# Kernel optimization log

Measured on AMD Instinct MI355X. Metric: run time of the kernel, lower is better.

The kernel has to match this reference:

```python
import jax, jax.numpy as jnp
import numpy as np


def exp_mix_frac(p1, p2, a1, b1, a2, b2):
    # stable merge of two (numerator, denominator) pairs carried in log-scale p
    p = jnp.maximum(p1, p2)
    e1 = jnp.exp(p1 - p)
    e2 = jnp.exp(p2 - p)
    return a1 * e1 + a2 * e2, b1 * e1 + b2 * e2, p


def assoc_reduce_step(left, right):
    akv_l, ak_l, w_l, p_l = left
    akv_r, ak_r, w_r, p_r = right
    a, b, p = exp_mix_frac(p_l + w_r, p_r, akv_l, ak_l, akv_r, ak_r)
    return a, b, w_l + w_r, p


def setup_inputs() -> dict:
    key = jax.random.key(0)
    ks = jax.random.split(key, 7)
    S, B, E = 2048, 8, 1024
    scale = 1.0 / np.sqrt(E)
    return {
        "x": jax.random.normal(ks[0], (S, B, E), jnp.float32),
        "tmrkv": jax.random.uniform(ks[1], (3 * E,), jnp.float32),
        "Wk": jax.random.normal(ks[2], (E, E), jnp.float32) * scale,
        "Wv": jax.random.normal(ks[3], (E, E), jnp.float32) * scale,
        "time_decay": jax.random.normal(ks[4], (E,), jnp.float32) - 1.0,
        "time_first": jax.random.normal(ks[5], (E,), jnp.float32),
        "Wout": jax.random.normal(ks[6], (E, E), jnp.float32) * scale,
    }


def reference(x, tmrkv, Wk, Wv, time_decay, time_first, Wout):
    # x: (S, B, E) time-major (batch_first=False path of the source module)
    S, B, E = x.shape
    x_prev = jnp.concatenate([jnp.zeros_like(x[:1]), x[:-1]], axis=0)
    # time_mix_rkv layout: [r | k | v]; r-branch is computed in the source but
    # never used in the associative-scan path, so it is omitted (same output).
    mk = tmrkv[E:2 * E]
    mv = tmrkv[2 * E:]
    k = (mk * x + (1.0 - mk) * x_prev) @ Wk  # (S, B, E)
    v = (mv * x + (1.0 - mv) * x_prev) @ Wv  # (S, B, E)

    k_ = k.reshape(S, B * E)
    v_ = v.reshape(S, B * E)
    W_ = jnp.broadcast_to(jnp.tile(time_decay, B)[None, :], (S, B * E))
    ones = jnp.ones_like(v_)
    # log-depth parallel scan over time with numerically-stable exp merge
    a_, b_, _, p_ = jax.lax.associative_scan(
        assoc_reduce_step, (v_, ones, W_, k_), axis=0)

    a_state = a_.reshape(S, B, E)
    b_state = b_.reshape(S, B, E)
    p_state = p_.reshape(S, B, E)
    c, d, _ = exp_mix_frac(p_state, k + time_first + time_decay,
                           a_state, b_state, v, jnp.ones_like(v))
    rwkv = c / d  # (S, B, E)
    return rwkv @ Wout
```

## Files before the change

### kernel.cpp

```cpp
#include <hip/hip_runtime.h>
#include <stdint.h>

#define S_LEN  2048
#define B_DIM  8
#define E_DIM  1024
#define BE     (B_DIM * E_DIM)
#define M_ROWS (S_LEN * B_DIM)
#define NCHUNK 64
#define CLEN   (S_LEN / NCHUNK)

typedef __attribute__((ext_vector_type(8))) short bf16x8;
typedef __attribute__((ext_vector_type(4))) float f32x4;

__device__ __forceinline__ unsigned short f2bf(float f) {
    unsigned int u = __float_as_uint(f);
    u += 0x7FFFu + ((u >> 16) & 1u);
    return (unsigned short)(u >> 16);
}
__device__ __forceinline__ float bf_lo(unsigned int u) {
    return __uint_as_float(u << 16);
}
__device__ __forceinline__ float bf_hi(unsigned int u) {
    return __uint_as_float(u & 0xFFFF0000u);
}

__global__ __launch_bounds__(256) void mix_kernel(
    const float* __restrict__ x, const float* __restrict__ tmrkv,
    unsigned short* __restrict__ xk, unsigned short* __restrict__ xv)
{
    int i = blockIdx.x * 256 + threadIdx.x;
    const float4* x4 = (const float4*)x;
    float4 xc[2], xp[2];
    xc[0] = x4[2 * i];
    xc[1] = x4[2 * i + 1];
    if (i >= BE / 8) {
        xp[0] = x4[2 * i - BE / 4];
        xp[1] = x4[2 * i + 1 - BE / 4];
    } else {
        xp[0] = make_float4(0.f, 0.f, 0.f, 0.f);
        xp[1] = make_float4(0.f, 0.f, 0.f, 0.f);
    }
    int e4 = (2 * i) & (E_DIM / 4 - 1);
    ushort4 ok[2], ov[2];
    #pragma unroll
    for (int h = 0; h < 2; ++h) {
        float4 mk = ((const float4*)(tmrkv + E_DIM))[e4 + h];
        float4 mv = ((const float4*)(tmrkv + 2 * E_DIM))[e4 + h];
        ok[h].x = f2bf(mk.x * xc[h].x + (1.f - mk.x) * xp[h].x);
        ok[h].y = f2bf(mk.y * xc[h].y + (1.f - mk.y) * xp[h].y);
        ok[h].z = f2bf(mk.z * xc[h].z + (1.f - mk.z) * xp[h].z);
        ok[h].w = f2bf(mk.w * xc[h].w + (1.f - mk.w) * xp[h].w);
        ov[h].x = f2bf(mv.x * xc[h].x + (1.f - mv.x) * xp[h].x);
        ov[h].y = f2bf(mv.y * xc[h].y + (1.f - mv.y) * xp[h].y);
        ov[h].z = f2bf(mv.z * xc[h].z + (1.f - mv.z) * xp[h].z);
        ov[h].w = f2bf(mv.w * xc[h].w + (1.f - mv.w) * xp[h].w);
    }
    ((ushort4*)xk)[2 * i]     = ok[0];
    ((ushort4*)xk)[2 * i + 1] = ok[1];
    ((ushort4*)xv)[2 * i]     = ov[0];
    ((ushort4*)xv)[2 * i + 1] = ov[1];
}

__global__ __launch_bounds__(256) void cast_transpose_k(
    const float* __restrict__ w0, const float* __restrict__ w1,
    const float* __restrict__ w2,
    unsigned short* __restrict__ o0, unsigned short* __restrict__ o1,
    unsigned short* __restrict__ o2)
{
    const float* in = blockIdx.z == 0 ? w0 : (blockIdx.z == 1 ? w1 : w2);
    unsigned short* out = blockIdx.z == 0 ? o0 : (blockIdx.z == 1 ? o1 : o2);
    __shared__ float tile[32][33];
    int bx = blockIdx.x * 32, by = blockIdx.y * 32;
    int tx = threadIdx.x, ty = threadIdx.y;
    #pragma unroll
    for (int i = 0; i < 32; i += 8)
        tile[ty + i][tx] = in[(size_t)(by + ty + i) * E_DIM + bx + tx];
    __syncthreads();
    #pragma unroll
    for (int i = 0; i < 32; i += 8)
        out[(size_t)(bx + ty + i) * E_DIM + by + tx] = f2bf(tile[tx][ty + i]);
}

#define BM 256
#define BN 256
#define BK 64

__device__ __forceinline__ void stage_plane(unsigned short* lds_base, int buf_plane,
                                            const unsigned short* gsrc, int K, int wave)
{
    #pragma unroll
    for (int s = 0; s < 2; ++s) {
        const unsigned short* g = gsrc + (size_t)s * 128 * K;
        unsigned short* l = lds_base + buf_plane * 8192 + s * 4096 + wave * 512;
        __builtin_amdgcn_global_load_lds(
            (const __attribute__((address_space(1))) unsigned int*)g,
            (__attribute__((address_space(3))) unsigned int*)l, 16, 0, 0);
    }
}

template <typename OutT>
__device__ __forceinline__ void gemm_body(
    const unsigned short* __restrict__ A,
    const unsigned short* __restrict__ BT,
    OutT* __restrict__ C, int M, int N, int K)
{
    __shared__ __align__(16) unsigned short smem[2][4][8192];
    const int tid  = threadIdx.x;
    const int wave = tid >> 6, lane = tid & 63;
    const int lrow = lane & 15, lq = lane >> 4;
    const int wm = wave >> 2, wn = wave & 3;
    const int bm = blockIdx.x * BM, bn = blockIdx.y * BN;

    const int srow = tid >> 2;
    const int sg   = (tid & 3) ^ ((srow >> 1) & 3);
    const unsigned short* sAp = A  + (size_t)(bm + srow) * K + sg * 8;
    const unsigned short* sBp = BT + (size_t)(bn + srow) * K + sg * 8;
    unsigned short* lb = &smem[0][0][0];

    f32x4 acc[8][4];
    #pragma unroll
    for (int i = 0; i < 8; ++i)
        #pragma unroll
        for (int j = 0; j < 4; ++j)
            acc[i][j] = (f32x4){0.f, 0.f, 0.f, 0.f};

    bf16x8 af[4], bfr[4];

#define LDA_(h, ib)                                                           \
    _Pragma("unroll")                                                         \
    for (int i = 0; i < 4; ++i) {                                             \
        int R = wm * 128 + ((ib) + i) * 16 + lrow;                            \
        af[i] = *(const bf16x8*)&smem[cur][(h) * 2]                           \
            [R * 32 + ((lq ^ ((R >> 1) & 3)) << 3)];                          \
    }
#define LDB_(h)                                                               \
    _Pragma("unroll")                                                         \
    for (int j = 0; j < 4; ++j) {                                             \
        int R = wn * 64 + j * 16 + lrow;                                      \
        bfr[j] = *(const bf16x8*)&smem[cur][(h) * 2 + 1]                      \
            [R * 32 + ((lq ^ ((R >> 1) & 3)) << 3)];                          \
    }
#define MMA_(ib)                                                              \
    __builtin_amdgcn_s_setprio(1);                                            \
    _Pragma("unroll")                                                         \
    for (int i = 0; i < 4; ++i)                                               \
        _Pragma("unroll")                                                     \
        for (int j = 0; j < 4; ++j)                                           \
            acc[(ib) + i][j] = __builtin_amdgcn_mfma_f32_16x16x32_bf16(       \
                af[i], bfr[j], acc[(ib) + i][j], 0, 0, 0);                    \
    __builtin_amdgcn_s_setprio(0);

    const int nk = K / BK;
    stage_plane(lb, 0, sAp,      K, wave);
    stage_plane(lb, 1, sBp,      K, wave);
    stage_plane(lb, 2, sAp + 32, K, wave);
    stage_plane(lb, 3, sBp + 32, K, wave);

    int cur = 0;
    for (int t = 0; t < nk - 1; ++t) {
        const int nxt = cur ^ 1;
        const unsigned short* nA = sAp + (size_t)(t + 1) * BK;
        const unsigned short* nB = sBp + (size_t)(t + 1) * BK;
        stage_plane(lb, nxt * 4 + 0, nA, K, wave);
        asm volatile("s_waitcnt vmcnt(6)" ::: "memory");
        __builtin_amdgcn_s_barrier();
        asm volatile("" ::: "memory");
        LDA_(0, 0); LDB_(0);
        MMA_(0);
        stage_plane(lb, nxt * 4 + 1, nB, K, wave);
        LDA_(0, 4);
        MMA_(4);
        stage_plane(lb, nxt * 4 + 2, nA + 32, K, wave);
        asm volatile("s_waitcnt vmcnt(6)" ::: "memory");
        __builtin_amdgcn_s_barrier();
        asm volatile("" ::: "memory");
        LDA_(1, 0); LDB_(1);
        MMA_(0);
        stage_plane(lb, nxt * 4 + 3, nB + 32, K, wave);
        LDA_(1, 4);
        asm volatile("s_waitcnt lgkmcnt(0)" ::: "memory");
        __builtin_amdgcn_s_barrier();
        asm volatile("" ::: "memory");
        MMA_(4);
        cur = nxt;
    }
    asm volatile("s_waitcnt vmcnt(4)" ::: "memory");
    __builtin_amdgcn_s_barrier();
    asm volatile("" ::: "memory");
    LDA_(0, 0); LDB_(0);
    MMA_(0);
    LDA_(0, 4);
    MMA_(4);
    asm volatile("s_waitcnt vmcnt(0)" ::: "memory");
    __builtin_amdgcn_s_barrier();
    asm volatile("" ::: "memory");
    LDA_(1, 0); LDB_(1);
    MMA_(0);
    LDA_(1, 4);
    MMA_(4);

    #pragma unroll
    for (int i = 0; i < 8; ++i)
        #pragma unroll
        for (int j = 0; j < 4; ++j)
            #pragma unroll
            for (int r = 0; r < 4; ++r) {
                int row = bm + wm * 128 + i * 16 + lq * 4 + r;
                int col = bn + wn * 64 + j * 16 + lrow;
                if constexpr (sizeof(OutT) == 2)
                    C[(size_t)row * N + col] = f2bf(acc[i][j][r]);
                else
                    C[(size_t)row * N + col] = acc[i][j][r];
            }
#undef LDA_
#undef LDB_
#undef MMA_
}

__global__ __launch_bounds__(512, 2) void gemm_kv(
    const unsigned short* __restrict__ A0, const unsigned short* __restrict__ B0,
    unsigned short* __restrict__ C0,
    const unsigned short* __restrict__ A1, const unsigned short* __restrict__ B1,
    unsigned short* __restrict__ C1, int M, int N, int K)
{
    if (blockIdx.z == 0) gemm_body<unsigned short>(A0, B0, C0, M, N, K);
    else                 gemm_body<unsigned short>(A1, B1, C1, M, N, K);
}

__global__ __launch_bounds__(512, 2) void gemm_out(
    const unsigned short* __restrict__ A, const unsigned short* __restrict__ BT,
    float* __restrict__ C, int M, int N, int K)
{
    gemm_body<float>(A, BT, C, M, N, K);
}

__device__ __forceinline__ void wkv_step(float& a, float& b, float& p,
                                         float kt, float vt, float w)
{
    float pw = p + w;
    float pn = fmaxf(pw, kt);
    float e1 = __expf(pw - pn), e2 = __expf(kt - pn);
    a = a * e1 + vt * e2;
    b = b * e1 + e2;
    p = pn;
}

#define Q_PER_T (BE / 4)

__global__ __launch_bounds__(256) void scan_pass1(
    const uint2* __restrict__ k4, const uint2* __restrict__ v4,
    const float* __restrict__ tdec,
    float4* __restrict__ sA, float4* __restrict__ sB, float4* __restrict__ sP)
{
    int g = blockIdx.x * 256 + threadIdx.x;
    int q = g & (Q_PER_T - 1);
    int c = g >> 11;
    float4 w4 = ((const float4*)tdec)[q & (E_DIM / 4 - 1)];
    size_t idx = (size_t)c * CLEN * Q_PER_T + q;
    uint2 ku = k4[idx], vu = v4[idx];
    float a0 = bf_lo(vu.x), b0 = 1.f, p0 = bf_lo(ku.x);
    float a1 = bf_hi(vu.x), b1 = 1.f, p1 = bf_hi(ku.x);
    float a2 = bf_lo(vu.y), b2 = 1.f, p2 = bf_lo(ku.y);
    float a3 = bf_hi(vu.y), b3 = 1.f, p3 = bf_hi(ku.y);
    for (int j = 1; j < CLEN; ++j) {
        idx += Q_PER_T;
        ku = k4[idx]; vu = v4[idx];
        wkv_step(a0, b0, p0, bf_lo(ku.x), bf_lo(vu.x), w4.x);
        wkv_step(a1, b1, p1, bf_hi(ku.x), bf_hi(vu.x), w4.y);
        wkv_step(a2, b2, p2, bf_lo(ku.y), bf_lo(vu.y), w4.z);
        wkv_step(a3, b3, p3, bf_hi(ku.y), bf_hi(vu.y), w4.w);
    }
    sA[g] = make_float4(a0, a1, a2, a3);
    sB[g] = make_float4(b0, b1, b2, b3);
    sP[g] = make_float4(p0, p1, p2, p3);
}

__global__ __launch_bounds__(256) void scan_pass2(
    const float* __restrict__ tdec,
    float* __restrict__ sA, float* __restrict__ sB, float* __restrict__ sP)
{
    __shared__ float tA[64 * 65], tB[64 * 65], tP[64 * 65];
    const int t   = threadIdx.x;
    const int ch0 = blockIdx.x * 64;
    const int chl = t & 63;
    const int cq  = t >> 6;
    #pragma unroll 4
    for (int cc = 0; cc < 16; ++cc) {
        int c = cq * 16 + cc;
        int idx = c * BE + ch0 + chl;
        tA[chl * 65 + c] = sA[idx];
        tB[chl * 65 + c] = sB[idx];
        tP[chl * 65 + c] = sP[idx];
    }
    __syncthreads();
    const int lane = t & 63, wave = t >> 6;
    for (int i = 0; i < 16; ++i) {
        int ch = wave * 16 + i;
        float w = tdec[(ch0 + ch) & (E_DIM - 1)];
        float a = tA[ch * 65 + lane];
        float b = tB[ch * 65 + lane];
        float p = tP[ch * 65 + lane];
        float W = (float)CLEN * w;
        #pragma unroll
        for (int d = 1; d < 64; d <<= 1) {
            float a_l = __shfl_up(a, d);
            float b_l = __shfl_up(b, d);
            float p_l = __shfl_up(p, d);
            float W_l = __shfl_up(W, d);
            if (lane >= d) {
                float pw = p_l + W;
                float pn = fmaxf(pw, p);
                float e1 = __expf(pw - pn), e2 = __expf(p - pn);
                a = a_l * e1 + a * e2;
                b = b_l * e1 + b * e2;
                p = pn;
                W = W_l + W;
            }
        }
        float ea = __shfl_up(a, 1);
        float eb = __shfl_up(b, 1);
        float ep = __shfl_up(p, 1);
        if (lane == 0) { ea = 0.f; eb = 0.f; ep = -__builtin_inff(); }
        tA[ch * 65 + lane] = ea;
        tB[ch * 65 + lane] = eb;
        tP[ch * 65 + lane] = ep;
    }
    __syncthreads();
    #pragma unroll 4
    for (int cc = 0; cc < 16; ++cc) {
        int c = cq * 16 + cc;
        int idx = c * BE + ch0 + chl;
        sA[idx] = tA[chl * 65 + c];
        sB[idx] = tB[chl * 65 + c];
        sP[idx] = tP[chl * 65 + c];
    }
}

__global__ __launch_bounds__(256) void scan_pass3(
    const uint2* __restrict__ k4, const uint2* __restrict__ v4,
    const float* __restrict__ tdec, const float* __restrict__ tfir,
    const float4* __restrict__ sA, const float4* __restrict__ sB,
    const float4* __restrict__ sP, uint2* __restrict__ rwkv4)
{
    int g = blockIdx.x * 256 + threadIdx.x;
    int q = g & (Q_PER_T - 1);
    int c = g >> 11;
    int e4 = q & (E_DIM / 4 - 1);
    float4 w4 = ((const float4*)tdec)[e4];
    float4 f4 = ((const float4*)tfir)[e4];
    float u0 = f4.x + w4.x, u1 = f4.y + w4.y;
    float u2 = f4.z + w4.z, u3 = f4.w + w4.w;
    float4 av = sA[g], bv = sB[g], pv = sP[g];
    float a0 = av.x, b0 = bv.x, p0 = pv.x;
    float a1 = av.y, b1 = bv.y, p1 = pv.y;
    float a2 = av.z, b2 = bv.z, p2 = pv.z;
    float a3 = av.w, b3 = bv.w, p3 = pv.w;
    size_t idx = (size_t)c * CLEN * Q_PER_T + q;
    for (int j = 0; j < CLEN; ++j) {
        uint2 ku = k4[idx], vu = v4[idx];
        float kt0 = bf_lo(ku.x), vt0 = bf_lo(vu.x);
        float kt1 = bf_hi(ku.x), vt1 = bf_hi(vu.x);
        float kt2 = bf_lo(ku.y), vt2 = bf_lo(vu.y);
        float kt3 = bf_hi(ku.y), vt3 = bf_hi(vu.y);
        wkv_step(a0, b0, p0, kt0, vt0, w4.x);
        wkv_step(a1, b1, p1, kt1, vt1, w4.y);
        wkv_step(a2, b2, p2, kt2, vt2, w4.z);
        wkv_step(a3, b3, p3, kt3, vt3, w4.w);
        float kb0 = kt0 + u0, kb1 = kt1 + u1, kb2 = kt2 + u2, kb3 = kt3 + u3;
        float q0 = fmaxf(p0, kb0), q1 = fmaxf(p1, kb1);
        float q2 = fmaxf(p2, kb2), q3 = fmaxf(p3, kb3);
        float g0 = __expf(p0 - q0), h0 = __expf(kb0 - q0);
        float g1 = __expf(p1 - q1), h1 = __expf(kb1 - q1);
        float g2 = __expf(p2 - q2), h2 = __expf(kb2 - q2);
        float g3 = __expf(p3 - q3), h3 = __expf(kb3 - q3);
        float r0 = (a0 * g0 + vt0 * h0) / (b0 * g0 + h0);
        float r1 = (a1 * g1 + vt1 * h1) / (b1 * g1 + h1);
        float r2 = (a2 * g2 + vt2 * h2) / (b2 * g2 + h2);
        float r3 = (a3 * g3 + vt3 * h3) / (b3 * g3 + h3);
        uint2 o;
        o.x = (unsigned int)f2bf(r0) | ((unsigned int)f2bf(r1) << 16);
        o.y = (unsigned int)f2bf(r2) | ((unsigned int)f2bf(r3) << 16);
        rwkv4[idx] = o;
        idx += Q_PER_T;
    }
}

extern "C" void kernel_launch(void* const* d_in, const int* in_sizes, int n_in,
                              void* d_out, int out_size, void* d_ws, size_t ws_size,
                              hipStream_t stream)
{
    const float* x     = (const float*)d_in[0];
    const float* tmrkv = (const float*)d_in[1];
    const float* Wk    = (const float*)d_in[2];
    const float* Wv    = (const float*)d_in[3];
    const float* tdec  = (const float*)d_in[4];
    const float* tfir  = (const float*)d_in[5];
    const float* Wout  = (const float*)d_in[6];
    float* out = (float*)d_out;

    char* ws = (char*)d_ws;
    const size_t SZ_BF = (size_t)M_ROWS * E_DIM * 2;
    unsigned short* xk   = (unsigned short*)(ws);
    unsigned short* xv   = (unsigned short*)(ws + SZ_BF);
    unsigned short* kbuf = (unsigned short*)(ws + 2 * SZ_BF);
    unsigned short* vbuf = (unsigned short*)(ws + 3 * SZ_BF);
    unsigned short* WkT  = (unsigned short*)(ws + 4 * SZ_BF);
    unsigned short* WvT  = WkT + (size_t)E_DIM * E_DIM;
    unsigned short* WoutT= WvT + (size_t)E_DIM * E_DIM;
    float* sA = (float*)xv;
    float* sB = sA + (size_t)NCHUNK * BE;
    float* sP = sB + (size_t)NCHUNK * BE;
    unsigned short* rwkv = xk;

    mix_kernel<<<(M_ROWS * E_DIM / 8) / 256, 256, 0, stream>>>(x, tmrkv, xk, xv);

    dim3 tb(32, 8), tg(E_DIM / 32, E_DIM / 32, 3);
    cast_transpose_k<<<tg, tb, 0, stream>>>(Wk, Wv, Wout, WkT, WvT, WoutT);

    dim3 gkv(M_ROWS / BM, E_DIM / BN, 2);
    gemm_kv<<<gkv, 512, 0, stream>>>(xk, WkT, kbuf, xv, WvT, vbuf,
                                     M_ROWS, E_DIM, E_DIM);

    scan_pass1<<<(NCHUNK * Q_PER_T) / 256, 256, 0, stream>>>(
        (const uint2*)kbuf, (const uint2*)vbuf, tdec,
        (float4*)sA, (float4*)sB, (float4*)sP);
    scan_pass2<<<BE / 64, 256, 0, stream>>>(tdec, sA, sB, sP);
    scan_pass3<<<(NCHUNK * Q_PER_T) / 256, 256, 0, stream>>>(
        (const uint2*)kbuf, (const uint2*)vbuf, tdec, tfir,
        (const float4*)sA, (const float4*)sB, (const float4*)sP,
        (uint2*)rwkv);

    dim3 gg(M_ROWS / BM, E_DIM / BN);
    gemm_out<<<gg, 512, 0, stream>>>(rwkv, WoutT, out, M_ROWS, E_DIM, E_DIM);
}
```

Baseline: 307.5 us.

## Switch GEMMs to 32x32x16 MFMA with XCD-aware block swizzle and reordered pipeline

The shared GEMM body now uses 32x32x16 bf16 MFMA instructions with 16-float accumulators instead of 16x16x32, which halves the number of LDS fragment loads per FLOP. The k-loop schedule is reordered so each gate (lgkm and vm wait plus barrier) comes before the LDS reads and the next-stage global loads are issued after them. Block indices are also remapped so that consecutive hardware block IDs on the same XCD cover neighbouring M tiles, which should improve L2 reuse. Together these aim to raise MFMA throughput and cache locality, at the cost of an extra full lgkmcnt wait per gate. The swizzle also hardcodes a grid of 64 M tiles per XCD group, which matches M=16384/256.

```diff
diff --git a/kernel.cpp b/kernel.cpp
--- a/kernel.cpp
+++ b/kernel.cpp
@@ -11,6 +11,7 @@
 
 typedef __attribute__((ext_vector_type(8))) short bf16x8;
 typedef __attribute__((ext_vector_type(4))) float f32x4;
+typedef __attribute__((ext_vector_type(16))) float f32x16;
 
 __device__ __forceinline__ unsigned short f2bf(float f) {
     unsigned int u = __float_as_uint(f);
@@ -98,18 +99,27 @@
     }
 }
 
+__device__ __forceinline__ void swz_xy(int& bx, int& by)
+{
+    int hw   = blockIdx.x + gridDim.x * blockIdx.y;
+    int xcd  = hw & 7;
+    int slot = hw >> 3;
+    bx = xcd * 8 + (slot & 7);
+    by = slot >> 3;
+}
+
 template <typename OutT>
 __device__ __forceinline__ void gemm_body(
     const unsigned short* __restrict__ A,
     const unsigned short* __restrict__ BT,
-    OutT* __restrict__ C, int M, int N, int K)
+    OutT* __restrict__ C, int M, int N, int K, int bxt, int byt)
 {
     __shared__ __align__(16) unsigned short smem[2][4][8192];
     const int tid  = threadIdx.x;
     const int wave = tid >> 6, lane = tid & 63;
-    const int lrow = lane & 15, lq = lane >> 4;
+    const int l31 = lane & 31, lh = lane >> 5;
     const int wm = wave >> 2, wn = wave & 3;
-    const int bm = blockIdx.x * BM, bn = blockIdx.y * BN;
+    const int bm = bxt * BM, bn = byt * BN;
 
     const int srow = tid >> 2;
     const int sg   = (tid & 3) ^ ((srow >> 1) & 3);
@@ -117,37 +127,55 @@
     const unsigned short* sBp = BT + (size_t)(bn + srow) * K + sg * 8;
     unsigned short* lb = &smem[0][0][0];
 
-    f32x4 acc[8][4];
-    #pragma unroll
-    for (int i = 0; i < 8; ++i)
+    f32x16 acc[4][2];
+    #pragma unroll
+    for (int i = 0; i < 4; ++i)
         #pragma unroll
-        for (int j = 0; j < 4; ++j)
-            acc[i][j] = (f32x4){0.f, 0.f, 0.f, 0.f};
-
-    bf16x8 af[4], bfr[4];
-
-#define LDA_(h, ib)                                                           \
+        for (int j = 0; j < 2; ++j)
+            #pragma unroll
+            for (int e = 0; e < 16; ++e)
+                acc[i][j][e] = 0.f;
+
+    bf16x8 af[2][2], bfr[2][2];
+
+#define GATE_(n)                                                              \
+    asm volatile("s_waitcnt lgkmcnt(0)" ::: "memory");                        \
+    asm volatile("s_waitcnt vmcnt(" #n ")" ::: "memory");                     \
+    __builtin_amdgcn_s_barrier();                                             \
+    asm volatile("" ::: "memory");
+
+#define LDA2_(h, mh)                                                          \
     _Pragma("unroll")                                                         \
-    for (int i = 0; i < 4; ++i) {                                             \
-        int R = wm * 128 + ((ib) + i) * 16 + lrow;                            \
-        af[i] = *(const bf16x8*)&smem[cur][(h) * 2]                           \
-            [R * 32 + ((lq ^ ((R >> 1) & 3)) << 3)];                          \
-    }
-#define LDB_(h)                                                               \
+    for (int ii = 0; ii < 2; ++ii)                                            \
+        _Pragma("unroll")                                                     \
+        for (int s = 0; s < 2; ++s) {                                         \
+            int R = wm * 128 + (2 * (mh) + ii) * 32 + l31;                    \
+            int g = s * 2 + lh;                                               \
+            af[ii][s] = *(const bf16x8*)&smem[cur][(h) * 2]                   \
+                [R * 32 + ((g ^ ((R >> 1) & 3)) << 3)];                       \
+        }
+#define LDB2_(h)                                                              \
     _Pragma("unroll")                                                         \
-    for (int j = 0; j < 4; ++j) {                                             \
-        int R = wn * 64 + j * 16 + lrow;                                      \
-        bfr[j] = *(const bf16x8*)&smem[cur][(h) * 2 + 1]                      \
-            [R * 32 + ((lq ^ ((R >> 1) & 3)) << 3)];                          \
-    }
-#define MMA_(ib)                                                              \
+    for (int jj = 0; jj < 2; ++jj)                                            \
+        _Pragma("unroll")                                                     \
+        for (int s = 0; s < 2; ++s) {                                         \
+            int R = wn * 64 + jj * 32 + l31;                                  \
+            int g = s * 2 + lh;                                               \
+            bfr[jj][s] = *(const bf16x8*)&smem[cur][(h) * 2 + 1]              \
+                [R * 32 + ((g ^ ((R >> 1) & 3)) << 3)];                       \
+        }
+#define MMA2_(mh)                                                             \
     __builtin_amdgcn_s_setprio(1);                                            \
     _Pragma("unroll")                                                         \
-    for (int i = 0; i < 4; ++i)                                               \
+    for (int ii = 0; ii < 2; ++ii)                                            \
         _Pragma("unroll")                                                     \
-        for (int j = 0; j < 4; ++j)                                           \
-            acc[(ib) + i][j] = __builtin_amdgcn_mfma_f32_16x16x32_bf16(       \
-                af[i], bfr[j], acc[(ib) + i][j], 0, 0, 0);                    \
+        for (int jj = 0; jj < 2; ++jj)                                        \
+            _Pragma("unroll")                                                 \
+            for (int s = 0; s < 2; ++s)                                       \
+                acc[2 * (mh) + ii][jj] =                                      \
+                    __builtin_amdgcn_mfma_f32_32x32x16_bf16(                  \
+                        af[ii][s], bfr[jj][s], acc[2 * (mh) + ii][jj],        \
+                        0, 0, 0);                                             \
     __builtin_amdgcn_s_setprio(0);
 
     const int nk = K / BK;
@@ -161,60 +189,50 @@
         const int nxt = cur ^ 1;
         const unsigned short* nA = sAp + (size_t)(t + 1) * BK;
         const unsigned short* nB = sBp + (size_t)(t + 1) * BK;
+        GATE_(4);
+        LDA2_(0, 0); LDB2_(0);
         stage_plane(lb, nxt * 4 + 0, nA, K, wave);
-        asm volatile("s_waitcnt vmcnt(6)" ::: "memory");
-        __builtin_amdgcn_s_barrier();
-        asm volatile("" ::: "memory");
-        LDA_(0, 0); LDB_(0);
-        MMA_(0);
+        MMA2_(0);
+        LDA2_(0, 1);
         stage_plane(lb, nxt * 4 + 1, nB, K, wave);
-        LDA_(0, 4);
-        MMA_(4);
+        MMA2_(1);
+        GATE_(4);
+        LDA2_(1, 0); LDB2_(1);
         stage_plane(lb, nxt * 4 + 2, nA + 32, K, wave);
-        asm volatile("s_waitcnt vmcnt(6)" ::: "memory");
-        __builtin_amdgcn_s_barrier();
-        asm volatile("" ::: "memory");
-        LDA_(1, 0); LDB_(1);
-        MMA_(0);
+        MMA2_(0);
+        LDA2_(1, 1);
         stage_plane(lb, nxt * 4 + 3, nB + 32, K, wave);
-        LDA_(1, 4);
-        asm volatile("s_waitcnt lgkmcnt(0)" ::: "memory");
-        __builtin_amdgcn_s_barrier();
-        asm volatile("" ::: "memory");
-        MMA_(4);
+        MMA2_(1);
         cur = nxt;
     }
-    asm volatile("s_waitcnt vmcnt(4)" ::: "memory");
-    __builtin_amdgcn_s_barrier();
-    asm volatile("" ::: "memory");
-    LDA_(0, 0); LDB_(0);
-    MMA_(0);
-    LDA_(0, 4);
-    MMA_(4);
-    asm volatile("s_waitcnt vmcnt(0)" ::: "memory");
-    __builtin_amdgcn_s_barrier();
-    asm volatile("" ::: "memory");
-    LDA_(1, 0); LDB_(1);
-    MMA_(0);
-    LDA_(1, 4);
-    MMA_(4);
-
-    #pragma unroll
-    for (int i = 0; i < 8; ++i)
+    GATE_(4);
+    LDA2_(0, 0); LDB2_(0);
+    MMA2_(0);
+    LDA2_(0, 1);
+    MMA2_(1);
+    GATE_(0);
+    LDA2_(1, 0); LDB2_(1);
+    MMA2_(0);
+    LDA2_(1, 1);
+    MMA2_(1);
+
+    #pragma unroll
+    for (int i = 0; i < 4; ++i)
         #pragma unroll
-        for (int j = 0; j < 4; ++j)
+        for (int j = 0; j < 2; ++j)
             #pragma unroll
-            for (int r = 0; r < 4; ++r) {
-                int row = bm + wm * 128 + i * 16 + lq * 4 + r;
-                int col = bn + wn * 64 + j * 16 + lrow;
+            for (int r = 0; r < 16; ++r) {
+                int row = bm + wm * 128 + i * 32 + (r & 3) + 8 * (r >> 2) + 4 * lh;
+                int col = bn + wn * 64 + j * 32 + l31;
                 if constexpr (sizeof(OutT) == 2)
                     C[(size_t)row * N + col] = f2bf(acc[i][j][r]);
                 else
                     C[(size_t)row * N + col] = acc[i][j][r];
             }
-#undef LDA_
-#undef LDB_
-#undef MMA_
+#undef GATE_
+#undef LDA2_
+#undef LDB2_
+#undef MMA2_
 }
 
 __global__ __launch_bounds__(512, 2) void gemm_kv(
@@ -223,15 +241,19 @@
     const unsigned short* __restrict__ A1, const unsigned short* __restrict__ B1,
     unsigned short* __restrict__ C1, int M, int N, int K)
 {
-    if (blockIdx.z == 0) gemm_body<unsigned short>(A0, B0, C0, M, N, K);
-    else                 gemm_body<unsigned short>(A1, B1, C1, M, N, K);
+    int bx, by;
+    swz_xy(bx, by);
+    if (blockIdx.z == 0) gemm_body<unsigned short>(A0, B0, C0, M, N, K, bx, by);
+    else                 gemm_body<unsigned short>(A1, B1, C1, M, N, K, bx, by);
 }
 
 __global__ __launch_bounds__(512, 2) void gemm_out(
     const unsigned short* __restrict__ A, const unsigned short* __restrict__ BT,
     float* __restrict__ C, int M, int N, int K)
 {
-    gemm_body<float>(A, BT, C, M, N, K);
+    int bx, by;
+    swz_xy(bx, by);
+    gemm_body<float>(A, BT, C, M, N, K, bx, by);
 }
 
 __device__ __forceinline__ void wkv_step(float& a, float& b, float& p,
```

Result: slower. 315.1 us (+2.5%).

## Halve GEMM K-tile, raise occupancy bound, and swizzle blocks across XCDs

Applied to the files above, without the earlier changes.

Reduces the GEMM K-step from 64 to 32, which halves the shared-memory double buffer and turns the pipeline into a simpler two-barrier loop per step. It raises the launch-bounds minimum to 4 blocks per CU to get more resident waves. It also remaps block indices so that neighbouring M tiles land on the same XCD, to improve L2 reuse. The occupancy bound caps registers at about 64 per lane, while the 8x4 f32x4 accumulator alone needs 128, so heavy spilling is a serious risk. The shorter K step also means more barriers per unit of MFMA work.

```diff
diff --git a/kernel.cpp b/kernel.cpp
--- a/kernel.cpp
+++ b/kernel.cpp
@@ -83,39 +83,48 @@
 
 #define BM 256
 #define BN 256
-#define BK 64
-
-__device__ __forceinline__ void stage_plane(unsigned short* lds_base, int buf_plane,
-                                            const unsigned short* gsrc, int K, int wave)
+#define BK 32
+
+__device__ __forceinline__ void stage_plane32(unsigned short* plane,
+                                              const unsigned short* gsrc,
+                                              int K, int wave)
 {
     #pragma unroll
     for (int s = 0; s < 2; ++s) {
         const unsigned short* g = gsrc + (size_t)s * 128 * K;
-        unsigned short* l = lds_base + buf_plane * 8192 + s * 4096 + wave * 512;
+        unsigned short* l = plane + s * 4096 + wave * 512;
         __builtin_amdgcn_global_load_lds(
             (const __attribute__((address_space(1))) unsigned int*)g,
             (__attribute__((address_space(3))) unsigned int*)l, 16, 0, 0);
     }
+}
+
+__device__ __forceinline__ void swz_xy(int& bx, int& by)
+{
+    int hw   = blockIdx.x + gridDim.x * blockIdx.y;
+    int xcd  = hw & 7;
+    int slot = hw >> 3;
+    bx = xcd * 8 + (slot & 7);
+    by = slot >> 3;
 }
 
 template <typename OutT>
 __device__ __forceinline__ void gemm_body(
     const unsigned short* __restrict__ A,
     const unsigned short* __restrict__ BT,
-    OutT* __restrict__ C, int M, int N, int K)
-{
-    __shared__ __align__(16) unsigned short smem[2][4][8192];
+    OutT* __restrict__ C, int M, int N, int K, int bxt, int byt)
+{
+    __shared__ __align__(16) unsigned short smem[2][2][8192];
     const int tid  = threadIdx.x;
     const int wave = tid >> 6, lane = tid & 63;
     const int lrow = lane & 15, lq = lane >> 4;
     const int wm = wave >> 2, wn = wave & 3;
-    const int bm = blockIdx.x * BM, bn = blockIdx.y * BN;
+    const int bm = bxt * BM, bn = byt * BN;
 
     const int srow = tid >> 2;
     const int sg   = (tid & 3) ^ ((srow >> 1) & 3);
     const unsigned short* sAp = A  + (size_t)(bm + srow) * K + sg * 8;
     const unsigned short* sBp = BT + (size_t)(bn + srow) * K + sg * 8;
-    unsigned short* lb = &smem[0][0][0];
 
     f32x4 acc[8][4];
     #pragma unroll
@@ -126,78 +135,59 @@
 
     bf16x8 af[4], bfr[4];
 
-#define LDA_(h, ib)                                                           \
+#define LDA_(ih)                                                              \
     _Pragma("unroll")                                                         \
     for (int i = 0; i < 4; ++i) {                                             \
-        int R = wm * 128 + ((ib) + i) * 16 + lrow;                            \
-        af[i] = *(const bf16x8*)&smem[cur][(h) * 2]                           \
+        int R = wm * 128 + ((ih) * 4 + i) * 16 + lrow;                        \
+        af[i] = *(const bf16x8*)&smem[cur][0]                                 \
             [R * 32 + ((lq ^ ((R >> 1) & 3)) << 3)];                          \
     }
-#define LDB_(h)                                                               \
+#define LDB_()                                                                \
     _Pragma("unroll")                                                         \
     for (int j = 0; j < 4; ++j) {                                             \
         int R = wn * 64 + j * 16 + lrow;                                      \
-        bfr[j] = *(const bf16x8*)&smem[cur][(h) * 2 + 1]                      \
+        bfr[j] = *(const bf16x8*)&smem[cur][1]                                \
             [R * 32 + ((lq ^ ((R >> 1) & 3)) << 3)];                          \
     }
-#define MMA_(ib)                                                              \
+#define MMA_(ih)                                                              \
     __builtin_amdgcn_s_setprio(1);                                            \
     _Pragma("unroll")                                                         \
     for (int i = 0; i < 4; ++i)                                               \
         _Pragma("unroll")                                                     \
         for (int j = 0; j < 4; ++j)                                           \
-            acc[(ib) + i][j] = __builtin_amdgcn_mfma_f32_16x16x32_bf16(       \
-                af[i], bfr[j], acc[(ib) + i][j], 0, 0, 0);                    \
+            acc[(ih) * 4 + i][j] = __builtin_amdgcn_mfma_f32_16x16x32_bf16(   \
+                af[i], bfr[j], acc[(ih) * 4 + i][j], 0, 0, 0);                \
     __builtin_amdgcn_s_setprio(0);
 
     const int nk = K / BK;
-    stage_plane(lb, 0, sAp,      K, wave);
-    stage_plane(lb, 1, sBp,      K, wave);
-    stage_plane(lb, 2, sAp + 32, K, wave);
-    stage_plane(lb, 3, sBp + 32, K, wave);
+    stage_plane32(&smem[0][0][0], sAp, K, wave);
+    stage_plane32(&smem[0][1][0], sBp, K, wave);
 
     int cur = 0;
-    for (int t = 0; t < nk - 1; ++t) {
-        const int nxt = cur ^ 1;
-        const unsigned short* nA = sAp + (size_t)(t + 1) * BK;
-        const unsigned short* nB = sBp + (size_t)(t + 1) * BK;
-        stage_plane(lb, nxt * 4 + 0, nA, K, wave);
-        asm volatile("s_waitcnt vmcnt(6)" ::: "memory");
-        __builtin_amdgcn_s_barrier();
-        asm volatile("" ::: "memory");
-        LDA_(0, 0); LDB_(0);
+    for (int t = 0; t < nk; ++t) {
+        if (t + 1 < nk) {
+            asm volatile("s_waitcnt lgkmcnt(0)" ::: "memory");
+            __builtin_amdgcn_s_barrier();
+            asm volatile("" ::: "memory");
+            stage_plane32(&smem[cur ^ 1][0][0], sAp + (size_t)(t + 1) * BK, K, wave);
+            stage_plane32(&smem[cur ^ 1][1][0], sBp + (size_t)(t + 1) * BK, K, wave);
+            asm volatile("s_waitcnt vmcnt(4)" ::: "memory");
+            __builtin_amdgcn_s_barrier();
+            asm volatile("" ::: "memory");
+        } else {
+            asm volatile("s_waitcnt lgkmcnt(0)" ::: "memory");
+            __builtin_amdgcn_s_barrier();
+            asm volatile("s_waitcnt vmcnt(0)" ::: "memory");
+            __builtin_amdgcn_s_barrier();
+            asm volatile("" ::: "memory");
+        }
+        LDB_();
+        LDA_(0);
         MMA_(0);
-        stage_plane(lb, nxt * 4 + 1, nB, K, wave);
-        LDA_(0, 4);
-        MMA_(4);
-        stage_plane(lb, nxt * 4 + 2, nA + 32, K, wave);
-        asm volatile("s_waitcnt vmcnt(6)" ::: "memory");
-        __builtin_amdgcn_s_barrier();
-        asm volatile("" ::: "memory");
-        LDA_(1, 0); LDB_(1);
-        MMA_(0);
-        stage_plane(lb, nxt * 4 + 3, nB + 32, K, wave);
-        LDA_(1, 4);
-        asm volatile("s_waitcnt lgkmcnt(0)" ::: "memory");
-        __builtin_amdgcn_s_barrier();
-        asm volatile("" ::: "memory");
-        MMA_(4);
-        cur = nxt;
-    }
-    asm volatile("s_waitcnt vmcnt(4)" ::: "memory");
-    __builtin_amdgcn_s_barrier();
-    asm volatile("" ::: "memory");
-    LDA_(0, 0); LDB_(0);
-    MMA_(0);
-    LDA_(0, 4);
-    MMA_(4);
-    asm volatile("s_waitcnt vmcnt(0)" ::: "memory");
-    __builtin_amdgcn_s_barrier();
-    asm volatile("" ::: "memory");
-    LDA_(1, 0); LDB_(1);
-    MMA_(0);
-    LDA_(1, 4);
-    MMA_(4);
+        LDA_(1);
+        MMA_(1);
+        cur ^= 1;
+    }
 
     #pragma unroll
     for (int i = 0; i < 8; ++i)
@@ -217,21 +207,25 @@
 #undef MMA_
 }
 
-__global__ __launch_bounds__(512, 2) void gemm_kv(
+__global__ __launch_bounds__(512, 4) void gemm_kv(
     const unsigned short* __restrict__ A0, const unsigned short* __restrict__ B0,
     unsigned short* __restrict__ C0,
     const unsigned short* __restrict__ A1, const unsigned short* __restrict__ B1,
     unsigned short* __restrict__ C1, int M, int N, int K)
 {
-    if (blockIdx.z == 0) gemm_body<unsigned short>(A0, B0, C0, M, N, K);
-    else                 gemm_body<unsigned short>(A1, B1, C1, M, N, K);
-}
-
-__global__ __launch_bounds__(512, 2) void gemm_out(
+    int bx, by;
+    swz_xy(bx, by);
+    if (blockIdx.z == 0) gemm_body<unsigned short>(A0, B0, C0, M, N, K, bx, by);
+    else                 gemm_body<unsigned short>(A1, B1, C1, M, N, K, bx, by);
+}
+
+__global__ __launch_bounds__(512, 4) void gemm_out(
     const unsigned short* __restrict__ A, const unsigned short* __restrict__ BT,
     float* __restrict__ C, int M, int N, int K)
 {
-    gemm_body<float>(A, BT, C, M, N, K);
+    int bx, by;
+    swz_xy(bx, by);
+    gemm_body<float>(A, BT, C, M, N, K, bx, by);
 }
 
 __device__ __forceinline__ void wkv_step(float& a, float& b, float& p,
```

Measured after the change: 1.042 ms. 239% more time.

## Restructure GEMM pipeline with uniform prefetch loop and XCD-aware block swizzle

Applied to the files above, without the earlier changes.

Folds the peeled last K-iteration into the main loop, guarding prefetches with a predicate, and moves each global->LDS stage to just after the LDS reads of its half. This changes where the barriers and waitcnts sit. Block indices are remapped so that consecutive hardware block IDs on the same XCD share M tiles, aiming for better L2 reuse. The occupancy hint of 2 is dropped from launch_bounds, which could change register allocation. The loop now waits lgkmcnt(0) before each barrier, which may reduce overlap. The swizzle hardcodes a grid of 64 blocks in x.

```diff
diff --git a/kernel.cpp b/kernel.cpp
--- a/kernel.cpp
+++ b/kernel.cpp
@@ -98,18 +98,27 @@
     }
 }
 
+__device__ __forceinline__ void swz_xy(int& bx, int& by)
+{
+    int hw   = blockIdx.x + gridDim.x * blockIdx.y;
+    int xcd  = hw & 7;
+    int slot = hw >> 3;
+    bx = xcd * 8 + (slot & 7);
+    by = slot >> 3;
+}
+
 template <typename OutT>
 __device__ __forceinline__ void gemm_body(
     const unsigned short* __restrict__ A,
     const unsigned short* __restrict__ BT,
-    OutT* __restrict__ C, int M, int N, int K)
+    OutT* __restrict__ C, int M, int N, int K, int bxt, int byt)
 {
     __shared__ __align__(16) unsigned short smem[2][4][8192];
     const int tid  = threadIdx.x;
     const int wave = tid >> 6, lane = tid & 63;
     const int lrow = lane & 15, lq = lane >> 4;
     const int wm = wave >> 2, wn = wave & 3;
-    const int bm = blockIdx.x * BM, bn = blockIdx.y * BN;
+    const int bm = bxt * BM, bn = byt * BN;
 
     const int srow = tid >> 2;
     const int sg   = (tid & 3) ^ ((srow >> 1) & 3);
@@ -157,47 +166,34 @@
     stage_plane(lb, 3, sBp + 32, K, wave);
 
     int cur = 0;
-    for (int t = 0; t < nk - 1; ++t) {
+    for (int t = 0; t < nk; ++t) {
         const int nxt = cur ^ 1;
         const unsigned short* nA = sAp + (size_t)(t + 1) * BK;
         const unsigned short* nB = sBp + (size_t)(t + 1) * BK;
-        stage_plane(lb, nxt * 4 + 0, nA, K, wave);
-        asm volatile("s_waitcnt vmcnt(6)" ::: "memory");
+        const bool pf = (t + 1 < nk);
+        asm volatile("s_waitcnt lgkmcnt(0)" ::: "memory");
+        asm volatile("s_waitcnt vmcnt(4)" ::: "memory");
         __builtin_amdgcn_s_barrier();
         asm volatile("" ::: "memory");
         LDA_(0, 0); LDB_(0);
+        if (pf) stage_plane(lb, nxt * 4 + 0, nA, K, wave);
         MMA_(0);
-        stage_plane(lb, nxt * 4 + 1, nB, K, wave);
         LDA_(0, 4);
+        if (pf) stage_plane(lb, nxt * 4 + 1, nB, K, wave);
         MMA_(4);
-        stage_plane(lb, nxt * 4 + 2, nA + 32, K, wave);
-        asm volatile("s_waitcnt vmcnt(6)" ::: "memory");
+        asm volatile("s_waitcnt lgkmcnt(0)" ::: "memory");
+        if (pf) { asm volatile("s_waitcnt vmcnt(4)" ::: "memory"); }
+        else    { asm volatile("s_waitcnt vmcnt(0)" ::: "memory"); }
         __builtin_amdgcn_s_barrier();
         asm volatile("" ::: "memory");
         LDA_(1, 0); LDB_(1);
+        if (pf) stage_plane(lb, nxt * 4 + 2, nA + 32, K, wave);
         MMA_(0);
-        stage_plane(lb, nxt * 4 + 3, nB + 32, K, wave);
         LDA_(1, 4);
-        asm volatile("s_waitcnt lgkmcnt(0)" ::: "memory");
-        __builtin_amdgcn_s_barrier();
-        asm volatile("" ::: "memory");
+        if (pf) stage_plane(lb, nxt * 4 + 3, nB + 32, K, wave);
         MMA_(4);
         cur = nxt;
     }
-    asm volatile("s_waitcnt vmcnt(4)" ::: "memory");
-    __builtin_amdgcn_s_barrier();
-    asm volatile("" ::: "memory");
-    LDA_(0, 0); LDB_(0);
-    MMA_(0);
-    LDA_(0, 4);
-    MMA_(4);
-    asm volatile("s_waitcnt vmcnt(0)" ::: "memory");
-    __builtin_amdgcn_s_barrier();
-    asm volatile("" ::: "memory");
-    LDA_(1, 0); LDB_(1);
-    MMA_(0);
-    LDA_(1, 4);
-    MMA_(4);
 
     #pragma unroll
     for (int i = 0; i < 8; ++i)
@@ -217,21 +213,25 @@
 #undef MMA_
 }
 
-__global__ __launch_bounds__(512, 2) void gemm_kv(
+__global__ __launch_bounds__(512) void gemm_kv(
     const unsigned short* __restrict__ A0, const unsigned short* __restrict__ B0,
     unsigned short* __restrict__ C0,
     const unsigned short* __restrict__ A1, const unsigned short* __restrict__ B1,
     unsigned short* __restrict__ C1, int M, int N, int K)
 {
-    if (blockIdx.z == 0) gemm_body<unsigned short>(A0, B0, C0, M, N, K);
-    else                 gemm_body<unsigned short>(A1, B1, C1, M, N, K);
-}
-
-__global__ __launch_bounds__(512, 2) void gemm_out(
+    int bx, by;
+    swz_xy(bx, by);
+    if (blockIdx.z == 0) gemm_body<unsigned short>(A0, B0, C0, M, N, K, bx, by);
+    else                 gemm_body<unsigned short>(A1, B1, C1, M, N, K, bx, by);
+}
+
+__global__ __launch_bounds__(512) void gemm_out(
     const unsigned short* __restrict__ A, const unsigned short* __restrict__ BT,
     float* __restrict__ C, int M, int N, int K)
 {
-    gemm_body<float>(A, BT, C, M, N, K);
+    int bx, by;
+    swz_xy(bx, by);
+    gemm_body<float>(A, BT, C, M, N, K, bx, by);
 }
 
 __device__ __forceinline__ void wkv_step(float& a, float& b, float& p,
```

Measured after the change: 309.5 us. No clear change (+0.6%).
